# Kernel tuning notes

Hardware: AMD Instinct MI355X
Metric: run time of the kernel (lower is better)

The kernel has to match this reference:

```python
import jax, jax.numpy as jnp
import numpy as np

NUM_EMBEDDINGS = 1024
EMBEDDING_DIM = 64
SCALE = 1.0 / NUM_EMBEDDINGS


def setup_inputs() -> dict:
    key = jax.random.key(0)
    k1, k2 = jax.random.split(key)
    input = jax.random.normal(k1, (16, EMBEDDING_DIM, 64, 64), dtype=jnp.float32)
    # nn.Embedding weight initialized uniform(-scale, scale)
    codebook = jax.random.uniform(k2, (NUM_EMBEDDINGS, EMBEDDING_DIM),
                                  dtype=jnp.float32, minval=-SCALE, maxval=SCALE)
    return {"input": input, "codebook": codebook}


def reference(input, codebook):
    # NCHW -> NHWC, flatten spatial+batch to tokens [N, D]
    x = jnp.transpose(input, (0, 2, 3, 1))           # [B, H, W, D]
    B, H, W, D = x.shape
    flat = x.reshape(-1, D)                          # [N, D]
    dists = (jnp.sum(flat ** 2, axis=1, keepdims=True)
             + jnp.sum(codebook ** 2, axis=1)
             - 2.0 * flat @ codebook.T)              # [N, K]
    idx = jnp.argmin(dists, axis=-1).reshape(B, H, W)  # [B, H, W]
    quantized = codebook[idx]                        # [B, H, W, D]
    return jnp.transpose(quantized, (0, 3, 1, 2))    # [B, D, H, W]
```

## Files before the change

### kernel.cpp

```cpp
#include <hip/hip_runtime.h>

typedef short short8 __attribute__((ext_vector_type(8)));
typedef float f32x4 __attribute__((ext_vector_type(4)));

#define NE 1024
#define D 64
#define HW 4096
#define NTOK 65536
#define MARGIN 4.0e-3f

#define WS_BN   0
#define WS_EBF  4096
#define WS_WIN  135168

__device__ __forceinline__ unsigned short f2bf(float f) {
    unsigned u = __float_as_uint(f);
    return (unsigned short)((u + 0x7fffu + ((u >> 16) & 1u)) >> 16);
}

__device__ __forceinline__ float np_sum64_sq(const float* v) {
    float s[8];
#pragma unroll
    for (int j = 0; j < 8; ++j) s[j] = __fmul_rn(v[j], v[j]);
#pragma unroll
    for (int i = 8; i < 64; i += 8) {
#pragma unroll
        for (int j = 0; j < 8; ++j)
            s[j] = __fadd_rn(s[j], __fmul_rn(v[i + j], v[i + j]));
    }
    return __fadd_rn(__fadd_rn(__fadd_rn(s[0], s[1]), __fadd_rn(s[2], s[3])),
                     __fadd_rn(__fadd_rn(s[4], s[5]), __fadd_rn(s[6], s[7])));
}

__global__ void k0_prep(const float* __restrict__ cb, float* __restrict__ bn,
                        unsigned short* __restrict__ ebf,
                        unsigned long long* __restrict__ mask) {
    int gid = blockIdx.x * 256 + threadIdx.x;
    ebf[gid] = f2bf(cb[gid]);
    int4 z = {0, 0, 0, 0};
    int4* mz = (int4*)mask;
#pragma unroll
    for (int i = 0; i < 8; ++i) mz[gid + i * 65536] = z;
    if (gid < NE) {
        float row[D];
        const float4* r4 = reinterpret_cast<const float4*>(cb + (size_t)gid * D);
#pragma unroll
        for (int i = 0; i < 16; ++i) {
            float4 v = r4[i];
            row[4*i+0] = v.x; row[4*i+1] = v.y; row[4*i+2] = v.z; row[4*i+3] = v.w;
        }
        bn[gid] = np_sum64_sq(row);
    }
}

__global__ __launch_bounds__(256) void k1_score(
        const float* __restrict__ in, const unsigned short* __restrict__ ebf,
        const float* __restrict__ bn_g, unsigned long long* __restrict__ mask) {
    __shared__ unsigned short ebq[256 * 64];
    __shared__ float sbn[NE];

    const int tid  = threadIdx.x;
    const int w    = tid >> 6;
    const int lane = tid & 63;
    const int lcol = lane & 15;
    const int lhi  = lane >> 4;
    const int lrow = lhi * 4;

    const int tokw = blockIdx.x * 128 + w * 32;
    const int b    = tokw >> 12;
    const int hwb  = tokw & 4095;

    for (int i = tid; i < NE; i += 256) sbn[i] = bn_g[i];

    const float* xbase = in + (size_t)b * (D * HW);
    short8 B00, B01, B10, B11;
    {
        const int hw0 = hwb + lcol, hw1 = hwb + 16 + lcol;
        const int kb  = lhi * 8;
        const float* p;
        p = xbase + (size_t)kb * HW + hw0;
#pragma unroll
        for (int j = 0; j < 8; ++j) B00[j] = (short)f2bf(p[(size_t)j * HW]);
        p = xbase + (size_t)(kb + 32) * HW + hw0;
#pragma unroll
        for (int j = 0; j < 8; ++j) B01[j] = (short)f2bf(p[(size_t)j * HW]);
        p = xbase + (size_t)kb * HW + hw1;
#pragma unroll
        for (int j = 0; j < 8; ++j) B10[j] = (short)f2bf(p[(size_t)j * HW]);
        p = xbase + (size_t)(kb + 32) * HW + hw1;
#pragma unroll
        for (int j = 0; j < 8; ++j) B11[j] = (short)f2bf(p[(size_t)j * HW]);
    }

    const int swz   = (lcol & 7) << 4;
    const int aoff0 = lcol * 128 + ((lhi * 16) ^ swz);
    const int aoff1 = lcol * 128 + ((64 + lhi * 16) ^ swz);

    float v10 = 3.402823466e+38f, v11 = 3.402823466e+38f;

    for (int q = 0; q < 4; ++q) {
        __syncthreads();
        const char* src = (const char*)ebf + q * 32768;
#pragma unroll
        for (int i = 0; i < 8; ++i) {
            int L = (tid + i * 256) * 16;
            int row = L >> 7, wi = L & 127;
            int4 v = *(const int4*)(src + L);
            *(int4*)((char*)ebq + row * 128 + (wi ^ ((row & 7) << 4))) = v;
        }
        __syncthreads();
#pragma unroll
        for (int ct = 0; ct < 16; ++ct) {
            const char* lp = (const char*)ebq + ct * 2048;
            short8 A0 = *(const short8*)(lp + aoff0);
            short8 A1 = *(const short8*)(lp + aoff1);
            f32x4 bnv = *(const f32x4*)(sbn + q * 256 + ct * 16 + lrow);
            f32x4 acc = {0.f, 0.f, 0.f, 0.f};
            acc = __builtin_amdgcn_mfma_f32_16x16x32_bf16(A0, B00, acc, 0, 0, 0);
            acc = __builtin_amdgcn_mfma_f32_16x16x32_bf16(A1, B01, acc, 0, 0, 0);
#pragma unroll
            for (int r = 0; r < 4; ++r)
                v10 = fminf(v10, __fmaf_rn(-2.0f, acc[r], bnv[r]));
            f32x4 ac2 = {0.f, 0.f, 0.f, 0.f};
            ac2 = __builtin_amdgcn_mfma_f32_16x16x32_bf16(A0, B10, ac2, 0, 0, 0);
            ac2 = __builtin_amdgcn_mfma_f32_16x16x32_bf16(A1, B11, ac2, 0, 0, 0);
#pragma unroll
            for (int r = 0; r < 4; ++r)
                v11 = fminf(v11, __fmaf_rn(-2.0f, ac2[r], bnv[r]));
        }
    }

    v10 = fminf(v10, __shfl_xor(v10, 16));
    v10 = fminf(v10, __shfl_xor(v10, 32));
    v11 = fminf(v11, __shfl_xor(v11, 16));
    v11 = fminf(v11, __shfl_xor(v11, 32));
    const float thr0 = v10 + MARGIN;
    const float thr1 = v11 + MARGIN;
    const unsigned int tokA = (unsigned)(tokw + lcol);
    const unsigned int tokB = tokA + 16u;

    for (int q = 0; q < 4; ++q) {
        __syncthreads();
        const char* src = (const char*)ebf + q * 32768;
#pragma unroll
        for (int i = 0; i < 8; ++i) {
            int L = (tid + i * 256) * 16;
            int row = L >> 7, wi = L & 127;
            int4 v = *(const int4*)(src + L);
            *(int4*)((char*)ebq + row * 128 + (wi ^ ((row & 7) << 4))) = v;
        }
        __syncthreads();
#pragma unroll
        for (int ct = 0; ct < 16; ++ct) {
            const char* lp = (const char*)ebq + ct * 2048;
            short8 A0 = *(const short8*)(lp + aoff0);
            short8 A1 = *(const short8*)(lp + aoff1);
            f32x4 bnv = *(const f32x4*)(sbn + q * 256 + ct * 16 + lrow);
            f32x4 acc = {0.f, 0.f, 0.f, 0.f};
            acc = __builtin_amdgcn_mfma_f32_16x16x32_bf16(A0, B00, acc, 0, 0, 0);
            acc = __builtin_amdgcn_mfma_f32_16x16x32_bf16(A1, B01, acc, 0, 0, 0);
            f32x4 ac2 = {0.f, 0.f, 0.f, 0.f};
            ac2 = __builtin_amdgcn_mfma_f32_16x16x32_bf16(A0, B10, ac2, 0, 0, 0);
            ac2 = __builtin_amdgcn_mfma_f32_16x16x32_bf16(A1, B11, ac2, 0, 0, 0);
            const int kub = q * 256 + ct * 16 + lrow;
#pragma unroll
            for (int r = 0; r < 4; ++r) {
                const int k = kub + r;
                float t0 = __fmaf_rn(-2.0f, acc[r], bnv[r]);
                if (t0 <= thr0)
                    atomicOr(&mask[(size_t)tokA * 16 + (k >> 6)], 1ull << (k & 63));
                float t1 = __fmaf_rn(-2.0f, ac2[r], bnv[r]);
                if (t1 <= thr1)
                    atomicOr(&mask[(size_t)tokB * 16 + (k >> 6)], 1ull << (k & 63));
            }
        }
    }
}

__global__ __launch_bounds__(256, 4) void k2_rerank(
        const float* __restrict__ in, const float* __restrict__ cb,
        const float* __restrict__ bn, const unsigned long long* __restrict__ mask,
        unsigned short* __restrict__ win) {
    const int tok = blockIdx.x * 256 + threadIdx.x;
    const int b = tok >> 12, hw = tok & 4095;
    const float* x = in + (size_t)b * (D * HW) + hw;
    float xv[D];
#pragma unroll
    for (int d = 0; d < D; ++d) xv[d] = x[(size_t)d * HW];
    const float a = np_sum64_sq(xv);

    float bestq = 3.402823466e+38f;
    int   bestk = 0;
    for (int wd = 0; wd < 16; ++wd) {
        unsigned long long m = mask[(size_t)tok * 16 + wd];
        while (m) {
            int bit = (int)__builtin_ctzll(m);
            m &= m - 1;
            int k = wd * 64 + bit;
            const float* er = cb + (size_t)k * D;
            float dot = 0.f;
#pragma unroll
            for (int d = 0; d < D; ++d) dot = __fmaf_rn(xv[d], er[d], dot);
            float qv = __fsub_rn(__fadd_rn(a, bn[k]), __fmul_rn(2.0f, dot));
            if (qv < bestq) { bestq = qv; bestk = k; }
        }
    }
    win[tok] = (unsigned short)bestk;
}

__global__ void k3_gather(const float* __restrict__ cb,
                          const unsigned short* __restrict__ win,
                          float* __restrict__ out) {
    const int tok = blockIdx.x * 256 + threadIdx.x;
    const int b = tok >> 12, hw = tok & 4095;
    const unsigned k = win[tok];
    float* ot = out + (size_t)b * (D * HW) + hw;
    const float4* er = reinterpret_cast<const float4*>(cb + (size_t)k * D);
#pragma unroll
    for (int i = 0; i < 16; ++i) {
        float4 e = er[i];
        ot[(size_t)(4*i+0) * HW] = e.x;
        ot[(size_t)(4*i+1) * HW] = e.y;
        ot[(size_t)(4*i+2) * HW] = e.z;
        ot[(size_t)(4*i+3) * HW] = e.w;
    }
}

extern "C" void kernel_launch(void* const* d_in, const int* in_sizes, int n_in,
                              void* d_out, int out_size, void* d_ws, size_t ws_size,
                              hipStream_t stream) {
    const float* in  = (const float*)d_in[0];
    const float* cb  = (const float*)d_in[1];
    float*       out = (float*)d_out;
    char*        ws  = (char*)d_ws;

    float*              bn   = (float*)(ws + WS_BN);
    unsigned short*     ebf  = (unsigned short*)(ws + WS_EBF);
    unsigned short*     win  = (unsigned short*)(ws + WS_WIN);
    unsigned long long* mask = (unsigned long long*)d_out;

    hipLaunchKernelGGL(k0_prep,   dim3(256), dim3(256), 0, stream, cb, bn, ebf, mask);
    hipLaunchKernelGGL(k1_score,  dim3(512), dim3(256), 0, stream, in, ebf, bn, mask);
    hipLaunchKernelGGL(k2_rerank, dim3(256), dim3(256), 0, stream, in, cb, bn, mask, win);
    hipLaunchKernelGGL(k3_gather, dim3(256), dim3(256), 0, stream, cb, win, out);
}
```

Measured before the change: 93.93 us.

## Split codebook scan across blocks and precompute bf16 input fragments

Input conversion to bf16 MFMA fragments moves into the prep kernel, which stores them in the spare half of the output buffer. The scoring kernel is split eight ways over the codebook, giving 4096 small blocks instead of 512 and aiming to raise occupancy and parallelism. Thresholds are now taken from each 128-code chunk's local minimum, so every token gets at least eight candidates. That adds atomics and rerank work, and the new single-candidate early exit in rerank will rarely fire.

```diff
diff --git a/kernel.cpp b/kernel.cpp
--- a/kernel.cpp
+++ b/kernel.cpp
@@ -8,10 +8,11 @@
 #define HW 4096
 #define NTOK 65536
 #define MARGIN 4.0e-3f
-
-#define WS_BN   0
-#define WS_EBF  4096
-#define WS_WIN  135168
+#define FLT_MAX_F 3.402823466e+38f
+
+#define WS_BN  0
+#define WS_EBF 4096
+#define WS_WIN 135168
 
 __device__ __forceinline__ unsigned short f2bf(float f) {
     unsigned u = __float_as_uint(f);
@@ -32,15 +33,19 @@
                      __fadd_rn(__fadd_rn(s[4], s[5]), __fadd_rn(s[6], s[7])));
 }
 
-__global__ void k0_prep(const float* __restrict__ cb, float* __restrict__ bn,
-                        unsigned short* __restrict__ ebf,
-                        unsigned long long* __restrict__ mask) {
-    int gid = blockIdx.x * 256 + threadIdx.x;
-    ebf[gid] = f2bf(cb[gid]);
-    int4 z = {0, 0, 0, 0};
-    int4* mz = (int4*)mask;
-#pragma unroll
-    for (int i = 0; i < 8; ++i) mz[gid + i * 65536] = z;
+__global__ __launch_bounds__(256) void kP_prep(
+        const float* __restrict__ in, const float* __restrict__ cb,
+        float* __restrict__ bn, unsigned short* __restrict__ ebf,
+        unsigned long long* __restrict__ mask, short8* __restrict__ frag) {
+    const int bid = blockIdx.x, tid = threadIdx.x;
+    const int gid = bid * 256 + tid;
+    {
+        int4 z = {0, 0, 0, 0};
+        int4* mz = (int4*)mask;
+#pragma unroll
+        for (int i = 0; i < 4; ++i) mz[(size_t)gid * 4 + i] = z;
+    }
+    if (gid < NE * D) ebf[gid] = f2bf(cb[gid]);
     if (gid < NE) {
         float row[D];
         const float4* r4 = reinterpret_cast<const float4*>(cb + (size_t)gid * D);
@@ -51,128 +56,103 @@
         }
         bn[gid] = np_sum64_sq(row);
     }
-}
-
-__global__ __launch_bounds__(256) void k1_score(
-        const float* __restrict__ in, const unsigned short* __restrict__ ebf,
-        const float* __restrict__ bn_g, unsigned long long* __restrict__ mask) {
-    __shared__ unsigned short ebq[256 * 64];
-    __shared__ float sbn[NE];
+    const int w = tid >> 6, lane = tid & 63, lcol = lane & 15, lhi = lane >> 4;
+    const int tokw = bid * 128 + w * 32;
+    const int b = tokw >> 12, hwb = tokw & 4095;
+    const float* xbase = in + (size_t)b * (D * HW);
+    const int hw0 = hwb + lcol, hw1 = hwb + 16 + lcol;
+    const int kb = lhi * 8;
+    short8 B00, B01, B10, B11;
+    const float* p;
+    p = xbase + (size_t)kb * HW + hw0;
+#pragma unroll
+    for (int j = 0; j < 8; ++j) B00[j] = (short)f2bf(p[(size_t)j * HW]);
+    p = xbase + (size_t)(kb + 32) * HW + hw0;
+#pragma unroll
+    for (int j = 0; j < 8; ++j) B01[j] = (short)f2bf(p[(size_t)j * HW]);
+    p = xbase + (size_t)kb * HW + hw1;
+#pragma unroll
+    for (int j = 0; j < 8; ++j) B10[j] = (short)f2bf(p[(size_t)j * HW]);
+    p = xbase + (size_t)(kb + 32) * HW + hw1;
+#pragma unroll
+    for (int j = 0; j < 8; ++j) B11[j] = (short)f2bf(p[(size_t)j * HW]);
+    short8* fp = frag + ((size_t)bid * 256 + tid) * 4;
+    fp[0] = B00; fp[1] = B01; fp[2] = B10; fp[3] = B11;
+}
+
+__global__ __launch_bounds__(256, 8) void k1_score(
+        const unsigned short* __restrict__ ebf, const float* __restrict__ bn_g,
+        const short8* __restrict__ frag, unsigned long long* __restrict__ mask) {
+    __shared__ unsigned short ebq[128 * 64];
+    __shared__ float sbn[128];
 
     const int tid  = threadIdx.x;
-    const int w    = tid >> 6;
-    const int lane = tid & 63;
-    const int lcol = lane & 15;
-    const int lhi  = lane >> 4;
-    const int lrow = lhi * 4;
-
-    const int tokw = blockIdx.x * 128 + w * 32;
-    const int b    = tokw >> 12;
-    const int hwb  = tokw & 4095;
-
-    for (int i = tid; i < NE; i += 256) sbn[i] = bn_g[i];
-
-    const float* xbase = in + (size_t)b * (D * HW);
-    short8 B00, B01, B10, B11;
-    {
-        const int hw0 = hwb + lcol, hw1 = hwb + 16 + lcol;
-        const int kb  = lhi * 8;
-        const float* p;
-        p = xbase + (size_t)kb * HW + hw0;
-#pragma unroll
-        for (int j = 0; j < 8; ++j) B00[j] = (short)f2bf(p[(size_t)j * HW]);
-        p = xbase + (size_t)(kb + 32) * HW + hw0;
-#pragma unroll
-        for (int j = 0; j < 8; ++j) B01[j] = (short)f2bf(p[(size_t)j * HW]);
-        p = xbase + (size_t)kb * HW + hw1;
-#pragma unroll
-        for (int j = 0; j < 8; ++j) B10[j] = (short)f2bf(p[(size_t)j * HW]);
-        p = xbase + (size_t)(kb + 32) * HW + hw1;
-#pragma unroll
-        for (int j = 0; j < 8; ++j) B11[j] = (short)f2bf(p[(size_t)j * HW]);
-    }
+    const int tg   = blockIdx.x >> 3;
+    const int c    = blockIdx.x & 7;
+    const int lane = tid & 63, w = tid >> 6;
+    const int lcol = lane & 15, lhi = lane >> 4, lrow = lhi * 4;
+    const int tokw = tg * 128 + w * 32;
+
+    if (tid < 128) sbn[tid] = bn_g[c * 128 + tid];
+    const char* src = (const char*)(ebf + (size_t)c * 128 * 64);
+#pragma unroll
+    for (int i = 0; i < 4; ++i) {
+        int L = (tid + i * 256) * 16;
+        int row = L >> 7, wi = L & 127;
+        int4 v = *(const int4*)(src + L);
+        *(int4*)((char*)ebq + row * 128 + (wi ^ ((row & 7) << 4))) = v;
+    }
+    const short8* fp = frag + ((size_t)tg * 256 + tid) * 4;
+    short8 B00 = fp[0], B01 = fp[1], B10 = fp[2], B11 = fp[3];
+    __syncthreads();
 
     const int swz   = (lcol & 7) << 4;
     const int aoff0 = lcol * 128 + ((lhi * 16) ^ swz);
     const int aoff1 = lcol * 128 + ((64 + lhi * 16) ^ swz);
 
-    float v10 = 3.402823466e+38f, v11 = 3.402823466e+38f;
-
-    for (int q = 0; q < 4; ++q) {
-        __syncthreads();
-        const char* src = (const char*)ebf + q * 32768;
-#pragma unroll
-        for (int i = 0; i < 8; ++i) {
-            int L = (tid + i * 256) * 16;
-            int row = L >> 7, wi = L & 127;
-            int4 v = *(const int4*)(src + L);
-            *(int4*)((char*)ebq + row * 128 + (wi ^ ((row & 7) << 4))) = v;
-        }
-        __syncthreads();
-#pragma unroll
-        for (int ct = 0; ct < 16; ++ct) {
-            const char* lp = (const char*)ebq + ct * 2048;
-            short8 A0 = *(const short8*)(lp + aoff0);
-            short8 A1 = *(const short8*)(lp + aoff1);
-            f32x4 bnv = *(const f32x4*)(sbn + q * 256 + ct * 16 + lrow);
-            f32x4 acc = {0.f, 0.f, 0.f, 0.f};
-            acc = __builtin_amdgcn_mfma_f32_16x16x32_bf16(A0, B00, acc, 0, 0, 0);
-            acc = __builtin_amdgcn_mfma_f32_16x16x32_bf16(A1, B01, acc, 0, 0, 0);
-#pragma unroll
-            for (int r = 0; r < 4; ++r)
-                v10 = fminf(v10, __fmaf_rn(-2.0f, acc[r], bnv[r]));
-            f32x4 ac2 = {0.f, 0.f, 0.f, 0.f};
-            ac2 = __builtin_amdgcn_mfma_f32_16x16x32_bf16(A0, B10, ac2, 0, 0, 0);
-            ac2 = __builtin_amdgcn_mfma_f32_16x16x32_bf16(A1, B11, ac2, 0, 0, 0);
-#pragma unroll
-            for (int r = 0; r < 4; ++r)
-                v11 = fminf(v11, __fmaf_rn(-2.0f, ac2[r], bnv[r]));
-        }
-    }
-
-    v10 = fminf(v10, __shfl_xor(v10, 16));
-    v10 = fminf(v10, __shfl_xor(v10, 32));
-    v11 = fminf(v11, __shfl_xor(v11, 16));
-    v11 = fminf(v11, __shfl_xor(v11, 32));
-    const float thr0 = v10 + MARGIN;
-    const float thr1 = v11 + MARGIN;
-    const unsigned int tokA = (unsigned)(tokw + lcol);
-    const unsigned int tokB = tokA + 16u;
-
-    for (int q = 0; q < 4; ++q) {
-        __syncthreads();
-        const char* src = (const char*)ebf + q * 32768;
-#pragma unroll
-        for (int i = 0; i < 8; ++i) {
-            int L = (tid + i * 256) * 16;
-            int row = L >> 7, wi = L & 127;
-            int4 v = *(const int4*)(src + L);
-            *(int4*)((char*)ebq + row * 128 + (wi ^ ((row & 7) << 4))) = v;
-        }
-        __syncthreads();
-#pragma unroll
-        for (int ct = 0; ct < 16; ++ct) {
-            const char* lp = (const char*)ebq + ct * 2048;
-            short8 A0 = *(const short8*)(lp + aoff0);
-            short8 A1 = *(const short8*)(lp + aoff1);
-            f32x4 bnv = *(const f32x4*)(sbn + q * 256 + ct * 16 + lrow);
-            f32x4 acc = {0.f, 0.f, 0.f, 0.f};
-            acc = __builtin_amdgcn_mfma_f32_16x16x32_bf16(A0, B00, acc, 0, 0, 0);
-            acc = __builtin_amdgcn_mfma_f32_16x16x32_bf16(A1, B01, acc, 0, 0, 0);
-            f32x4 ac2 = {0.f, 0.f, 0.f, 0.f};
-            ac2 = __builtin_amdgcn_mfma_f32_16x16x32_bf16(A0, B10, ac2, 0, 0, 0);
-            ac2 = __builtin_amdgcn_mfma_f32_16x16x32_bf16(A1, B11, ac2, 0, 0, 0);
-            const int kub = q * 256 + ct * 16 + lrow;
-#pragma unroll
-            for (int r = 0; r < 4; ++r) {
-                const int k = kub + r;
-                float t0 = __fmaf_rn(-2.0f, acc[r], bnv[r]);
-                if (t0 <= thr0)
-                    atomicOr(&mask[(size_t)tokA * 16 + (k >> 6)], 1ull << (k & 63));
-                float t1 = __fmaf_rn(-2.0f, ac2[r], bnv[r]);
-                if (t1 <= thr1)
-                    atomicOr(&mask[(size_t)tokB * 16 + (k >> 6)], 1ull << (k & 63));
-            }
+    float v10 = FLT_MAX_F, v11 = FLT_MAX_F;
+#pragma unroll
+    for (int ct = 0; ct < 8; ++ct) {
+        const char* lp = (const char*)ebq + ct * 2048;
+        short8 A0 = *(const short8*)(lp + aoff0);
+        short8 A1 = *(const short8*)(lp + aoff1);
+        f32x4 bnv = *(const f32x4*)(sbn + ct * 16 + lrow);
+        f32x4 acc = {0.f, 0.f, 0.f, 0.f};
+        acc = __builtin_amdgcn_mfma_f32_16x16x32_bf16(A0, B00, acc, 0, 0, 0);
+        acc = __builtin_amdgcn_mfma_f32_16x16x32_bf16(A1, B01, acc, 0, 0, 0);
+#pragma unroll
+        for (int r = 0; r < 4; ++r) v10 = fminf(v10, __fmaf_rn(-2.0f, acc[r], bnv[r]));
+        f32x4 ac2 = {0.f, 0.f, 0.f, 0.f};
+        ac2 = __builtin_amdgcn_mfma_f32_16x16x32_bf16(A0, B10, ac2, 0, 0, 0);
+        ac2 = __builtin_amdgcn_mfma_f32_16x16x32_bf16(A1, B11, ac2, 0, 0, 0);
+#pragma unroll
+        for (int r = 0; r < 4; ++r) v11 = fminf(v11, __fmaf_rn(-2.0f, ac2[r], bnv[r]));
+    }
+    v10 = fminf(v10, __shfl_xor(v10, 16)); v10 = fminf(v10, __shfl_xor(v10, 32));
+    v11 = fminf(v11, __shfl_xor(v11, 16)); v11 = fminf(v11, __shfl_xor(v11, 32));
+    const float thr0 = v10 + MARGIN, thr1 = v11 + MARGIN;
+    unsigned long long* mrow0 = mask + (size_t)(tokw + lcol) * 16;
+    unsigned long long* mrow1 = mask + (size_t)(tokw + 16 + lcol) * 16;
+
+#pragma unroll
+    for (int ct = 0; ct < 8; ++ct) {
+        const char* lp = (const char*)ebq + ct * 2048;
+        short8 A0 = *(const short8*)(lp + aoff0);
+        short8 A1 = *(const short8*)(lp + aoff1);
+        f32x4 bnv = *(const f32x4*)(sbn + ct * 16 + lrow);
+        f32x4 acc = {0.f, 0.f, 0.f, 0.f};
+        acc = __builtin_amdgcn_mfma_f32_16x16x32_bf16(A0, B00, acc, 0, 0, 0);
+        acc = __builtin_amdgcn_mfma_f32_16x16x32_bf16(A1, B01, acc, 0, 0, 0);
+        f32x4 ac2 = {0.f, 0.f, 0.f, 0.f};
+        ac2 = __builtin_amdgcn_mfma_f32_16x16x32_bf16(A0, B10, ac2, 0, 0, 0);
+        ac2 = __builtin_amdgcn_mfma_f32_16x16x32_bf16(A1, B11, ac2, 0, 0, 0);
+        const int kg = c * 128 + ct * 16 + lrow;
+#pragma unroll
+        for (int r = 0; r < 4; ++r) {
+            float t0 = __fmaf_rn(-2.0f, acc[r], bnv[r]);
+            if (t0 <= thr0) atomicOr(&mrow0[(kg + r) >> 6], 1ull << ((kg + r) & 63));
+            float t1 = __fmaf_rn(-2.0f, ac2[r], bnv[r]);
+            if (t1 <= thr1) atomicOr(&mrow1[(kg + r) >> 6], 1ull << ((kg + r) & 63));
         }
     }
 }
@@ -183,19 +163,33 @@
         unsigned short* __restrict__ win) {
     const int tok = blockIdx.x * 256 + threadIdx.x;
     const int b = tok >> 12, hw = tok & 4095;
+
+    unsigned long long m[16];
+    int tot = 0;
+#pragma unroll
+    for (int i = 0; i < 16; ++i) { m[i] = mask[(size_t)tok * 16 + i]; tot += (int)__popcll(m[i]); }
+    if (tot == 1) {
+        int kk = 0;
+#pragma unroll
+        for (int i = 0; i < 16; ++i) if (m[i]) kk = i * 64 + (int)__builtin_ctzll(m[i]);
+        win[tok] = (unsigned short)kk;
+        return;
+    }
+
     const float* x = in + (size_t)b * (D * HW) + hw;
     float xv[D];
 #pragma unroll
     for (int d = 0; d < D; ++d) xv[d] = x[(size_t)d * HW];
     const float a = np_sum64_sq(xv);
 
-    float bestq = 3.402823466e+38f;
+    float bestq = FLT_MAX_F;
     int   bestk = 0;
+#pragma unroll
     for (int wd = 0; wd < 16; ++wd) {
-        unsigned long long m = mask[(size_t)tok * 16 + wd];
-        while (m) {
-            int bit = (int)__builtin_ctzll(m);
-            m &= m - 1;
+        unsigned long long mm = m[wd];
+        while (mm) {
+            int bit = (int)__builtin_ctzll(mm);
+            mm &= mm - 1;
             int k = wd * 64 + bit;
             const float* er = cb + (size_t)k * D;
             float dot = 0.f;
@@ -238,9 +232,10 @@
     unsigned short*     ebf  = (unsigned short*)(ws + WS_EBF);
     unsigned short*     win  = (unsigned short*)(ws + WS_WIN);
     unsigned long long* mask = (unsigned long long*)d_out;
-
-    hipLaunchKernelGGL(k0_prep,   dim3(256), dim3(256), 0, stream, cb, bn, ebf, mask);
-    hipLaunchKernelGGL(k1_score,  dim3(512), dim3(256), 0, stream, in, ebf, bn, mask);
-    hipLaunchKernelGGL(k2_rerank, dim3(256), dim3(256), 0, stream, in, cb, bn, mask, win);
-    hipLaunchKernelGGL(k3_gather, dim3(256), dim3(256), 0, stream, cb, win, out);
-}
+    short8*             frag = (short8*)((char*)d_out + 8388608);
+
+    hipLaunchKernelGGL(kP_prep,   dim3(512),  dim3(256), 0, stream, in, cb, bn, ebf, mask, frag);
+    hipLaunchKernelGGL(k1_score,  dim3(4096), dim3(256), 0, stream, ebf, bn, frag, mask);
+    hipLaunchKernelGGL(k2_rerank, dim3(256),  dim3(256), 0, stream, in, cb, bn, mask, win);
+    hipLaunchKernelGGL(k3_gather, dim3(256),  dim3(256), 0, stream, cb, win, out);
+}
```

Measured after the change: 185.1 us. +97.1%, slower.
